# Performance work log

Hardware: AMD Instinct MI355X
Metric: run time of the kernel (lower is better)

## Reference

```python
import jax, jax.numpy as jnp
import numpy as np
from math import sqrt

B, N, M, HID, NH = 16, 512, 1024, 512, 8
HS = HID // NH  # 64


def layer_norm(x, g, b, eps=1e-5):
    mu = jnp.mean(x, axis=-1, keepdims=True)
    var = jnp.var(x, axis=-1, keepdims=True)
    return (x - mu) * jax.lax.rsqrt(var + eps) * g + b


def apply_moverz(x, s, c):
    # x: [B, L, NH, HS]; s, c: [B, L, 1, HS//2]
    x0, x1 = x[..., 0::2], x[..., 1::2]
    return jnp.concatenate([x0 * c - x1 * s, x1 * c + x0 * s], axis=-1)


def attention(q, k, v, mask):
    # q: [B,Nq,NH,HS], k/v: [B,Nk,NH,HS], mask broadcastable to [B,NH,Nq,Nk]
    attn = jnp.einsum('bnhd,bmhd->bhnm', q, k) / sqrt(HS)
    attn = jnp.where(mask, -jnp.inf, attn)
    attn = jax.nn.softmax(attn, axis=-1)
    x = jnp.einsum('bhnm,bmhd->bnhd', attn, v)
    return x.reshape(x.shape[0], x.shape[1], HID)


def setup_inputs() -> dict:
    key = jax.random.key(0)
    ks = jax.random.split(key, 24)
    inp = {}
    inp['tgt'] = jax.random.normal(ks[0], (B, N, HID), dtype=jnp.float32)
    inp['mem'] = jax.random.normal(ks[1], (B, M, HID), dtype=jnp.float32)
    th_p = jax.random.uniform(ks[2], (B, N, 1, HS // 2), dtype=jnp.float32) * (2 * np.pi)
    th_k = jax.random.uniform(ks[3], (B, M, 1, HS // 2), dtype=jnp.float32) * (2 * np.pi)
    inp['pep_mass_sin'] = jnp.sin(th_p)
    inp['pep_mass_cos'] = jnp.cos(th_p)
    inp['peaks_moverz_sin'] = jnp.sin(th_k)
    inp['peaks_moverz_cos'] = jnp.cos(th_k)
    # causal self-attn mask (True = masked)
    inp['tgt_mask'] = jnp.triu(jnp.ones((N, N), dtype=bool), k=1)[None, None]
    # pad last 64 memory positions
    pad = jnp.arange(M) >= (M - 64)
    inp['mem_key_padding_mask'] = jnp.broadcast_to(pad[None, None, None, :], (B, 1, 1, M))
    s = 0.02
    w = lambda i, shape: jax.random.normal(ks[i], shape, dtype=jnp.float32) * s
    # MaskedMultiHeadAttn params
    inp['mmha_w'] = w(4, (3 * HID, HID)); inp['mmha_b'] = jnp.zeros((3 * HID,), jnp.float32)
    inp['mmha_ow'] = w(5, (HID, HID)); inp['mmha_ob'] = jnp.zeros((HID,), jnp.float32)
    inp['mmha_g'] = jnp.ones((HID,), jnp.float32); inp['mmha_beta'] = jnp.zeros((HID,), jnp.float32)
    # MultiHeadAttn (cross) params
    inp['mha_qw'] = w(6, (HID, HID)); inp['mha_qb'] = jnp.zeros((HID,), jnp.float32)
    inp['mha_kvw'] = w(7, (2 * HID, HID)); inp['mha_kvb'] = jnp.zeros((2 * HID,), jnp.float32)
    inp['mha_ow'] = w(8, (HID, HID)); inp['mha_ob'] = jnp.zeros((HID,), jnp.float32)
    inp['mha_g'] = jnp.ones((HID,), jnp.float32); inp['mha_beta'] = jnp.zeros((HID,), jnp.float32)
    # FFN params (no bias)
    inp['ffn_w1'] = w(9, (4 * HID, HID))
    inp['ffn_w2'] = w(10, (HID, 4 * HID))
    inp['ffn_g'] = jnp.ones((HID,), jnp.float32); inp['ffn_beta'] = jnp.zeros((HID,), jnp.float32)
    return inp


def reference(tgt, mem, pep_mass_sin, pep_mass_cos, peaks_moverz_sin, peaks_moverz_cos,
              tgt_mask, mem_key_padding_mask,
              mmha_w, mmha_b, mmha_ow, mmha_ob, mmha_g, mmha_beta,
              mha_qw, mha_qb, mha_kvw, mha_kvb, mha_ow, mha_ob, mha_g, mha_beta,
              ffn_w1, ffn_w2, ffn_g, ffn_beta):
    # --- masked self-attention ---
    qkv = (tgt @ mmha_w.T + mmha_b).reshape(B, N, NH, 3 * HS)
    q, k, v = jnp.split(qkv, 3, axis=-1)
    x = attention(q, k, v, tgt_mask)
    tgt = layer_norm(x @ mmha_ow.T + mmha_ob + tgt, mmha_g, mmha_beta)
    # --- cross-attention with moverz distance bias ---
    q = (tgt @ mha_qw.T + mha_qb).reshape(B, N, NH, HS)
    q = apply_moverz(q, pep_mass_sin, pep_mass_cos)
    kv = (mem @ mha_kvw.T + mha_kvb).reshape(B, M, NH, 2 * HS)
    k, v = jnp.split(kv, 2, axis=-1)
    k = apply_moverz(k, peaks_moverz_sin, peaks_moverz_cos)
    x = attention(q, k, v, mem_key_padding_mask)
    tgt = layer_norm(x @ mha_ow.T + mha_ob + tgt, mha_g, mha_beta)
    # --- FFN ---
    h = jax.nn.relu(tgt @ ffn_w1.T) @ ffn_w2.T
    tgt = layer_norm(tgt + h, ffn_g, ffn_beta)
    return tgt
```

## Files before the change

kernel.cpp:

```cpp
#include <hip/hip_runtime.h>
#include <hip/hip_bf16.h>

#define BB 16
#define NN 512
#define MM 1024
#define HIDD 512
#define NHH 8

typedef unsigned short ushort_t;
typedef __attribute__((ext_vector_type(8))) short short8;
typedef __attribute__((ext_vector_type(8))) _Float16 half8;
typedef __attribute__((ext_vector_type(4))) _Float16 half4;
typedef __attribute__((ext_vector_type(4))) float f32x4;

__device__ __forceinline__ ushort_t f2bf(float x) {
    unsigned u = __float_as_uint(x);
    u += 0x7fff + ((u >> 16) & 1);
    return (ushort_t)(u >> 16);
}

#define GLD16(g, l) __builtin_amdgcn_global_load_lds(                      \
    (const __attribute__((address_space(1))) void*)(g),                    \
    (__attribute__((address_space(3))) void*)(l), 16, 0, 0)

__device__ __forceinline__ void xcd_swizzle(int& colb, int& rowb) {
    int id = blockIdx.x + blockIdx.y * gridDim.x;
    int C = gridDim.x;
    int xcd = id & 7;
    int slot = id >> 3;
    int rows_per = gridDim.y >> 3;
    colb = slot % C;
    rowb = xcd * rows_per + slot / C;
}

__global__ __launch_bounds__(256)
void gemm_bf(const ushort_t* __restrict__ A, const ushort_t* __restrict__ W,
             const float* __restrict__ bias, float* __restrict__ C,
             ushort_t* __restrict__ Cb, _Float16* __restrict__ Ch,
             int K, int Cout, int relu) {
    __shared__ __align__(16) ushort_t smem[2][8192];
    const int tid = threadIdx.x;
    const int lane = tid & 63;
    const int wid = tid >> 6;
    const int wm = wid >> 1, wn = wid & 1;
    int colb, rowb;
    xcd_swizzle(colb, rowb);
    const long row0 = (long)rowb * 128;
    const long col0 = (long)colb * 128;

    const int sr = lane >> 2;
    const int skq = lane & 3;
    const ushort_t* Ag = A + (row0 + wid * 32 + sr) * (long)K + skq * 8;
    const ushort_t* Wg = W + (col0 + wid * 32 + sr) * (long)K + skq * 8;
    const int sa0 = (wid * 32) * 32, sa1 = (wid * 32 + 16) * 32;

    f32x4 acc[4][4] = {};
    const int lr = lane & 15;
    const int kg = lane >> 4;

    GLD16(Ag, &smem[0][sa0]);
    GLD16(Ag + 16 * (long)K, &smem[0][sa1]);
    GLD16(Wg, &smem[0][4096 + sa0]);
    GLD16(Wg + 16 * (long)K, &smem[0][4096 + sa1]);

    int pb = 0;
    for (int k0 = 0; k0 < K; k0 += 32, pb ^= 1) {
        __syncthreads();
        int kn = k0 + 32;
        if (kn < K) {
            GLD16(Ag + kn, &smem[pb ^ 1][sa0]);
            GLD16(Ag + 16 * (long)K + kn, &smem[pb ^ 1][sa1]);
            GLD16(Wg + kn, &smem[pb ^ 1][4096 + sa0]);
            GLD16(Wg + 16 * (long)K + kn, &smem[pb ^ 1][4096 + sa1]);
        }
        const ushort_t* Ab = smem[pb];
        const ushort_t* Wb = smem[pb] + 4096;
        short8 af[4], bfr[4];
#pragma unroll
        for (int i = 0; i < 4; i++)
            af[i] = *(const short8*)&Ab[(wm * 64 + i * 16 + lr) * 32 + kg * 8];
#pragma unroll
        for (int j = 0; j < 4; j++)
            bfr[j] = *(const short8*)&Wb[(wn * 64 + j * 16 + lr) * 32 + kg * 8];
#pragma unroll
        for (int i = 0; i < 4; i++)
#pragma unroll
            for (int j = 0; j < 4; j++)
                acc[i][j] = __builtin_amdgcn_mfma_f32_16x16x32_bf16(
                    af[i], bfr[j], acc[i][j], 0, 0, 0);
    }

#pragma unroll
    for (int i = 0; i < 4; i++) {
#pragma unroll
        for (int j = 0; j < 4; j++) {
            long row = row0 + wm * 64 + i * 16 + kg * 4;
            long col = col0 + wn * 64 + j * 16 + lr;
            float bv = bias ? bias[col] : 0.f;
#pragma unroll
            for (int r = 0; r < 4; r++) {
                float x = acc[i][j][r] + bv;
                if (relu) x = fmaxf(x, 0.f);
                size_t idx = (row + r) * (size_t)Cout + col;
                if (Ch)      Ch[idx] = (_Float16)x;
                else if (Cb) Cb[idx] = f2bf(x);
                else         C[idx] = x;
            }
        }
    }
}

__global__ __launch_bounds__(256)
void gemm_bf64(const ushort_t* __restrict__ A, const ushort_t* __restrict__ W,
               const float* __restrict__ bias, float* __restrict__ C,
               ushort_t* __restrict__ Cb, _Float16* __restrict__ Ch,
               int K, int Cout, int relu) {
    __shared__ __align__(16) ushort_t smem[2][6144];
    const int tid = threadIdx.x;
    const int lane = tid & 63;
    const int w = tid >> 6;
    int colb, rowb;
    xcd_swizzle(colb, rowb);
    const long row0 = (long)rowb * 128;
    const long col0 = (long)colb * 64;

    const int sr = lane >> 2;
    const int skq = lane & 3;
    const ushort_t* Ag = A + (row0 + w * 32 + sr) * (long)K + skq * 8;
    const ushort_t* Wg = W + (col0 + w * 16 + sr) * (long)K + skq * 8;
    const int sa0 = (w * 32) * 32, sa1 = (w * 32 + 16) * 32;
    const int sw0 = 4096 + (w * 16) * 32;

    f32x4 acc[2][4] = {};
    const int lr = lane & 15;
    const int kg = lane >> 4;

    GLD16(Ag, &smem[0][sa0]);
    GLD16(Ag + 16 * (long)K, &smem[0][sa1]);
    GLD16(Wg, &smem[0][sw0]);

    int pb = 0;
    for (int k0 = 0; k0 < K; k0 += 32, pb ^= 1) {
        __syncthreads();
        int kn = k0 + 32;
        if (kn < K) {
            GLD16(Ag + kn, &smem[pb ^ 1][sa0]);
            GLD16(Ag + 16 * (long)K + kn, &smem[pb ^ 1][sa1]);
            GLD16(Wg + kn, &smem[pb ^ 1][sw0]);
        }
        const ushort_t* Ab = smem[pb];
        const ushort_t* Wb = smem[pb] + 4096;
        short8 af[2], bfr[4];
#pragma unroll
        for (int i = 0; i < 2; i++)
            af[i] = *(const short8*)&Ab[(w * 32 + i * 16 + lr) * 32 + kg * 8];
#pragma unroll
        for (int j = 0; j < 4; j++)
            bfr[j] = *(const short8*)&Wb[(j * 16 + lr) * 32 + kg * 8];
#pragma unroll
        for (int i = 0; i < 2; i++)
#pragma unroll
            for (int j = 0; j < 4; j++)
                acc[i][j] = __builtin_amdgcn_mfma_f32_16x16x32_bf16(
                    af[i], bfr[j], acc[i][j], 0, 0, 0);
    }

#pragma unroll
    for (int i = 0; i < 2; i++) {
#pragma unroll
        for (int j = 0; j < 4; j++) {
            long row = row0 + w * 32 + i * 16 + kg * 4;
            long col = col0 + j * 16 + lr;
            float bv = bias ? bias[col] : 0.f;
#pragma unroll
            for (int r = 0; r < 4; r++) {
                float x = acc[i][j][r] + bv;
                if (relu) x = fmaxf(x, 0.f);
                size_t idx = (row + r) * (size_t)Cout + col;
                if (Ch)      Ch[idx] = (_Float16)x;
                else if (Cb) Cb[idx] = f2bf(x);
                else         C[idx] = x;
            }
        }
    }
}

__global__ __launch_bounds__(256)
void gemm_q_rot(const ushort_t* __restrict__ A, const ushort_t* __restrict__ W,
                const float* __restrict__ bias,
                const float* __restrict__ sn, const float* __restrict__ cs,
                _Float16* __restrict__ Qrot) {
    __shared__ __align__(16) ushort_t smem[2][6144];
    _Float16* Cs = (_Float16*)smem;
    const int K = 512;
    const int tid = threadIdx.x;
    const int lane = tid & 63;
    const int w = tid >> 6;
    int colb, rowb;
    xcd_swizzle(colb, rowb);
    const long row0 = (long)rowb * 128;
    const int h = colb;
    const long col0 = (long)h * 64;

    const int sr = lane >> 2;
    const int skq = lane & 3;
    const ushort_t* Ag = A + (row0 + w * 32 + sr) * (long)K + skq * 8;
    const ushort_t* Wg = W + (col0 + w * 16 + sr) * (long)K + skq * 8;
    const int sa0 = (w * 32) * 32, sa1 = (w * 32 + 16) * 32;
    const int sw0 = 4096 + (w * 16) * 32;

    f32x4 acc[2][4] = {};
    const int lr = lane & 15;
    const int kg = lane >> 4;

    GLD16(Ag, &smem[0][sa0]);
    GLD16(Ag + 16 * (long)K, &smem[0][sa1]);
    GLD16(Wg, &smem[0][sw0]);

    int pb = 0;
    for (int k0 = 0; k0 < K; k0 += 32, pb ^= 1) {
        __syncthreads();
        int kn = k0 + 32;
        if (kn < K) {
            GLD16(Ag + kn, &smem[pb ^ 1][sa0]);
            GLD16(Ag + 16 * (long)K + kn, &smem[pb ^ 1][sa1]);
            GLD16(Wg + kn, &smem[pb ^ 1][sw0]);
        }
        const ushort_t* Ab = smem[pb];
        const ushort_t* Wb = smem[pb] + 4096;
        short8 af[2], bfr[4];
#pragma unroll
        for (int i = 0; i < 2; i++)
            af[i] = *(const short8*)&Ab[(w * 32 + i * 16 + lr) * 32 + kg * 8];
#pragma unroll
        for (int j = 0; j < 4; j++)
            bfr[j] = *(const short8*)&Wb[(j * 16 + lr) * 32 + kg * 8];
#pragma unroll
        for (int i = 0; i < 2; i++)
#pragma unroll
            for (int j = 0; j < 4; j++)
                acc[i][j] = __builtin_amdgcn_mfma_f32_16x16x32_bf16(
                    af[i], bfr[j], acc[i][j], 0, 0, 0);
    }

    __syncthreads();
#pragma unroll
    for (int i = 0; i < 2; i++)
#pragma unroll
        for (int j = 0; j < 4; j++) {
            int row = w * 32 + i * 16 + kg * 4;
            int col = j * 16 + lr;
            float bv = bias[col0 + col];
#pragma unroll
            for (int r = 0; r < 4; r++)
                Cs[(row + r) * 76 + col] = (_Float16)(acc[i][j][r] + bv);
        }
    __syncthreads();
    for (int idx = tid; idx < 4096; idx += 256) {
        int rr = idx >> 5, j = idx & 31;
        size_t srow = (size_t)row0 + rr;
        float x0 = (float)Cs[rr * 76 + 2 * j], x1 = (float)Cs[rr * 76 + 2 * j + 1];
        float s = sn[srow * 32 + j], c = cs[srow * 32 + j];
        Qrot[srow * 512 + h * 64 + j]      = (_Float16)(x0 * c - x1 * s);
        Qrot[srow * 512 + h * 64 + 32 + j] = (_Float16)(x1 * c + x0 * s);
    }
}

__global__ __launch_bounds__(256)
void gemm_kv(const ushort_t* __restrict__ A, const ushort_t* __restrict__ W,
             const float* __restrict__ bias,
             const float* __restrict__ sn, const float* __restrict__ cs,
             _Float16* __restrict__ Krot, _Float16* __restrict__ Vth) {
    __shared__ __align__(16) ushort_t smem[2][8192];
    _Float16* Cs = (_Float16*)smem;
    const int K = 512;
    const int tid = threadIdx.x;
    const int lane = tid & 63;
    const int wid = tid >> 6;
    const int wm = wid >> 1, wn = wid & 1;
    int colb, rowb;
    xcd_swizzle(colb, rowb);
    const long row0 = (long)rowb * 128;
    const int h = colb;
    const long col0 = (long)h * 128;

    const int sr = lane >> 2;
    const int skq = lane & 3;
    const ushort_t* Ag = A + (row0 + wid * 32 + sr) * (long)K + skq * 8;
    const ushort_t* Wg = W + (col0 + wid * 32 + sr) * (long)K + skq * 8;
    const int sa0 = (wid * 32) * 32, sa1 = (wid * 32 + 16) * 32;

    f32x4 acc[4][4] = {};
    const int lr = lane & 15;
    const int kg = lane >> 4;

    GLD16(Ag, &smem[0][sa0]);
    GLD16(Ag + 16 * (long)K, &smem[0][sa1]);
    GLD16(Wg, &smem[0][4096 + sa0]);
    GLD16(Wg + 16 * (long)K, &smem[0][4096 + sa1]);

    int pb = 0;
    for (int k0 = 0; k0 < K; k0 += 32, pb ^= 1) {
        __syncthreads();
        int kn = k0 + 32;
        if (kn < K) {
            GLD16(Ag + kn, &smem[pb ^ 1][sa0]);
            GLD16(Ag + 16 * (long)K + kn, &smem[pb ^ 1][sa1]);
            GLD16(Wg + kn, &smem[pb ^ 1][4096 + sa0]);
            GLD16(Wg + 16 * (long)K + kn, &smem[pb ^ 1][4096 + sa1]);
        }
        const ushort_t* Ab = smem[pb];
        const ushort_t* Wb = smem[pb] + 4096;
        short8 af[4], bfr[4];
#pragma unroll
        for (int i = 0; i < 4; i++)
            af[i] = *(const short8*)&Ab[(wm * 64 + i * 16 + lr) * 32 + kg * 8];
#pragma unroll
        for (int j = 0; j < 4; j++)
            bfr[j] = *(const short8*)&Wb[(wn * 64 + j * 16 + lr) * 32 + kg * 8];
#pragma unroll
        for (int i = 0; i < 4; i++)
#pragma unroll
            for (int j = 0; j < 4; j++)
                acc[i][j] = __builtin_amdgcn_mfma_f32_16x16x32_bf16(
                    af[i], bfr[j], acc[i][j], 0, 0, 0);
    }

    const int b_ = (int)(row0 >> 10);
    const int m0_ = (int)(row0 & 1023);
#pragma unroll
    for (int half = 0; half < 2; half++) {
        __syncthreads();
        if (wn == half) {
#pragma unroll
            for (int i = 0; i < 4; i++)
#pragma unroll
                for (int j = 0; j < 4; j++) {
                    int row = wm * 64 + i * 16 + kg * 4;
                    int col = j * 16 + lr;
                    float bv = bias[col0 + half * 64 + col];
#pragma unroll
                    for (int r = 0; r < 4; r++)
                        Cs[(row + r) * 76 + col] = (_Float16)(acc[i][j][r] + bv);
                }
        }
        __syncthreads();
        if (half == 0) {
            for (int idx = tid; idx < 4096; idx += 256) {
                int rr = idx >> 5, j = idx & 31;
                size_t srow = (size_t)row0 + rr;
                float x0 = (float)Cs[rr * 76 + 2 * j], x1 = (float)Cs[rr * 76 + 2 * j + 1];
                float s = sn[srow * 32 + j], c = cs[srow * 32 + j];
                Krot[srow * 512 + h * 64 + j]      = (_Float16)(x0 * c - x1 * s);
                Krot[srow * 512 + h * 64 + 32 + j] = (_Float16)(x1 * c + x0 * s);
            }
        } else {
            for (int idx = tid; idx < 1024; idx += 256) {
                int d = idx >> 4, c = idx & 15;
                half8 v;
#pragma unroll
                for (int k = 0; k < 8; k++) v[k] = Cs[(c * 8 + k) * 76 + d];
                *(half8*)(Vth + (((size_t)(b_ * NHH + h)) * 64 + d) * MM
                          + m0_ + c * 8) = v;
            }
        }
    }
}

__global__ __launch_bounds__(256)
void cvt_all(const float* __restrict__ tgt, const float* __restrict__ mem,
             const float* __restrict__ w0, const float* __restrict__ w1,
             const float* __restrict__ w2, const float* __restrict__ w3,
             const float* __restrict__ w4, const float* __restrict__ w5,
             const float* __restrict__ w6,
             ushort_t* __restrict__ Abf, ushort_t* __restrict__ membf,
             ushort_t* __restrict__ Wbf) {
    int blk = blockIdx.x;
    const float* src;
    ushort_t* dst;
    size_t off;
    if (blk < 4096)       { src = tgt; dst = Abf;   off = (size_t)blk * 1024; }
    else if (blk < 12288) { src = mem; dst = membf; off = (size_t)(blk - 4096) * 1024; }
    else {
        int wb = blk - 12288;
        dst = Wbf + (size_t)wb * 1024;
        if (wb < 768)       { src = w0; off = (size_t)wb * 1024; }
        else if (wb < 1024) { src = w1; off = (size_t)(wb - 768) * 1024; }
        else if (wb < 1280) { src = w2; off = (size_t)(wb - 1024) * 1024; }
        else if (wb < 1792) { src = w3; off = (size_t)(wb - 1280) * 1024; }
        else if (wb < 2048) { src = w4; off = (size_t)(wb - 1792) * 1024; }
        else if (wb < 3072) { src = w5; off = (size_t)(wb - 2048) * 1024; }
        else                { src = w6; off = (size_t)(wb - 3072) * 1024; }
        float4 v = *(const float4*)(src + off + threadIdx.x * 4);
        ushort4 o;
        o.x = f2bf(v.x); o.y = f2bf(v.y); o.z = f2bf(v.z); o.w = f2bf(v.w);
        *(ushort4*)(dst + threadIdx.x * 4) = o;
        return;
    }
    float4 v = *(const float4*)(src + off + threadIdx.x * 4);
    ushort4 o;
    o.x = f2bf(v.x); o.y = f2bf(v.y); o.z = f2bf(v.z); o.w = f2bf(v.w);
    *(ushort4*)(dst + off + threadIdx.x * 4) = o;
}

__global__ __launch_bounds__(256)
void prep_vt(const _Float16* __restrict__ src, int L, int stride,
             int hmul, int hadd, _Float16* __restrict__ Vt) {
    const int b = blockIdx.z, h = blockIdx.y, m0 = blockIdx.x * 64;
    const int tid = threadIdx.x;
    __shared__ _Float16 vt[64][72];
    for (int idx = tid; idx < 512; idx += 256) {
        int m = idx >> 3, c = idx & 7;
        half8 v = *(const half8*)(src + ((size_t)(b * L + m0 + m)) * stride
                                  + h * hmul + hadd + c * 8);
#pragma unroll
        for (int k = 0; k < 8; k++) vt[c * 8 + k][m] = v[k];
    }
    __syncthreads();
    for (int idx = tid; idx < 512; idx += 256) {
        int d = idx >> 3, c = idx & 7;
        *(half8*)(Vt + (((size_t)(b * NHH + h)) * 64 + d) * L + m0 + c * 8)
            = *(const half8*)&vt[d][c * 8];
    }
}

__global__ __launch_bounds__(256)
void attn7(const _Float16* __restrict__ Q, int qstride, int qmul, int qadd,
           const _Float16* __restrict__ K, int kstride, int kmul, int kadd,
           const _Float16* __restrict__ Vt, int LV, int Lrows,
           ushort_t* __restrict__ out, int kvlen, int causal) {
    const int g = blockIdx.x;
    const int bh = (g & 7) * 16 + ((g >> 3) & 15);
    const int qb = g >> 7;
    const int b = bh >> 3, h = bh & 7;
    const int n0 = qb * 128;
    const int tid = threadIdx.x, lane = tid & 63, w = tid >> 6;
    const int quad = lane >> 4, l16 = lane & 15;
    const int qw = n0 + w * 32;

    __shared__ _Float16 Ks[64 * 64];
    __shared__ _Float16 Vs[64 * 64];
    __shared__ _Float16 Ps[4][32 * 64];
    _Float16* Pw = Ps[w];

    half8 bq[2][2];
#pragma unroll
    for (int s = 0; s < 2; s++)
#pragma unroll
        for (int c = 0; c < 2; c++)
            bq[s][c] = *(const half8*)(Q + ((size_t)(b * NN + qw + s * 16 + l16)) * qstride
                                       + h * qmul + qadd + c * 32 + quad * 8);

    f32x4 acc[2][4] = {};
    float mrun[2] = {-3e38f, -3e38f}, lrun[2] = {0.f, 0.f};

    const int srow = tid >> 3;
    const int scol = tid & 7;
    const int ssw = (scol ^ (srow & 7)) * 8;
    const int limit = causal ? (n0 + 128) : kvlen;

    half8 kr0, kr1, vr0, vr1;
    {
        size_t kb = ((size_t)(b * Lrows + srow)) * kstride + h * kmul + kadd + scol * 8;
        kr0 = *(const half8*)(K + kb);
        kr1 = *(const half8*)(K + kb + (size_t)32 * kstride);
        size_t vb = (((size_t)(b * NHH + h)) * 64 + srow) * (size_t)LV + scol * 8;
        vr0 = *(const half8*)(Vt + vb);
        vr1 = *(const half8*)(Vt + vb + (size_t)32 * LV);
    }

    const int fsw = l16 & 7;
    for (int key0 = 0; key0 < limit; key0 += 64) {
        __syncthreads();
        *(half8*)&Ks[srow * 64 + ssw] = kr0;
        *(half8*)&Ks[(srow + 32) * 64 + ssw] = kr1;
        *(half8*)&Vs[srow * 64 + ssw] = vr0;
        *(half8*)&Vs[(srow + 32) * 64 + ssw] = vr1;
        __syncthreads();
        int knext = key0 + 64;
        if (knext < limit) {
            size_t kb = ((size_t)(b * Lrows + knext + srow)) * kstride
                        + h * kmul + kadd + scol * 8;
            kr0 = *(const half8*)(K + kb);
            kr1 = *(const half8*)(K + kb + (size_t)32 * kstride);
            size_t vb = (((size_t)(b * NHH + h)) * 64 + srow) * (size_t)LV
                        + knext + scol * 8;
            vr0 = *(const half8*)(Vt + vb);
            vr1 = *(const half8*)(Vt + vb + (size_t)32 * LV);
        }
        if (causal && key0 > qw + 31) continue;

        f32x4 st[2][4];
#pragma unroll
        for (int kt = 0; kt < 4; kt++) {
            const int rk = kt * 16 + l16;
            half8 ak0 = *(const half8*)&Ks[rk * 64 + ((quad ^ fsw) * 8)];
            half8 ak1 = *(const half8*)&Ks[rk * 64 + (((quad + 4) ^ fsw) * 8)];
#pragma unroll
            for (int s = 0; s < 2; s++) {
                f32x4 z = {};
                z = __builtin_amdgcn_mfma_f32_16x16x32_f16(ak0, bq[s][0], z, 0, 0, 0);
                z = __builtin_amdgcn_mfma_f32_16x16x32_f16(ak1, bq[s][1], z, 0, 0, 0);
                st[s][kt] = z;
            }
        }
        if (causal && key0 + 64 > qw) {
#pragma unroll
            for (int s = 0; s < 2; s++) {
                int qabs = qw + s * 16 + l16;
#pragma unroll
                for (int kt = 0; kt < 4; kt++)
#pragma unroll
                    for (int r = 0; r < 4; r++)
                        if (key0 + kt * 16 + quad * 4 + r > qabs)
                            st[s][kt][r] = -3e38f;
            }
        }
#pragma unroll
        for (int s = 0; s < 2; s++) {
            float lm = -3e38f;
#pragma unroll
            for (int kt = 0; kt < 4; kt++)
                lm = fmaxf(lm, fmaxf(fmaxf(st[s][kt][0], st[s][kt][1]),
                                     fmaxf(st[s][kt][2], st[s][kt][3])));
            lm = fmaxf(lm, __shfl_xor(lm, 16));
            lm = fmaxf(lm, __shfl_xor(lm, 32));
            float mnew = fmaxf(mrun[s], lm);
            float corr = __expf((mrun[s] - mnew) * 0.125f);
            mrun[s] = mnew;
            float ls = 0.f;
            const int rp = s * 16 + l16;
#pragma unroll
            for (int kt = 0; kt < 4; kt++) {
                half4 ph;
#pragma unroll
                for (int r = 0; r < 4; r++) {
                    float p = __expf((st[s][kt][r] - mnew) * 0.125f);
                    ls += p;
                    ph[r] = (_Float16)p;
                }
                int jc = 2 * kt + (quad >> 1);
                *(half4*)&Pw[rp * 64 + ((jc ^ fsw) * 8) + (quad & 1) * 4] = ph;
            }
            ls += __shfl_xor(ls, 16);
            ls += __shfl_xor(ls, 32);
            lrun[s] = lrun[s] * corr + ls;
            float cb0 = __shfl(corr, (lane & 48) | (quad * 4 + 0));
            float cb1 = __shfl(corr, (lane & 48) | (quad * 4 + 1));
            float cb2 = __shfl(corr, (lane & 48) | (quad * 4 + 2));
            float cb3 = __shfl(corr, (lane & 48) | (quad * 4 + 3));
#pragma unroll
            for (int dt = 0; dt < 4; dt++) {
                acc[s][dt][0] *= cb0; acc[s][dt][1] *= cb1;
                acc[s][dt][2] *= cb2; acc[s][dt][3] *= cb3;
            }
        }
        half8 ap[2][2];
#pragma unroll
        for (int s = 0; s < 2; s++) {
            const int rp = s * 16 + l16;
#pragma unroll
            for (int c = 0; c < 2; c++)
                ap[s][c] = *(const half8*)&Pw[rp * 64 + (((c * 4 + quad) ^ fsw) * 8)];
        }
#pragma unroll
        for (int dt = 0; dt < 4; dt++) {
            const int rv = dt * 16 + l16;
            half8 bv0 = *(const half8*)&Vs[rv * 64 + ((quad ^ fsw) * 8)];
            half8 bv1 = *(const half8*)&Vs[rv * 64 + (((quad + 4) ^ fsw) * 8)];
#pragma unroll
            for (int s = 0; s < 2; s++) {
                acc[s][dt] = __builtin_amdgcn_mfma_f32_16x16x32_f16(ap[s][0], bv0, acc[s][dt], 0, 0, 0);
                acc[s][dt] = __builtin_amdgcn_mfma_f32_16x16x32_f16(ap[s][1], bv1, acc[s][dt], 0, 0, 0);
            }
        }
    }
#pragma unroll
    for (int s = 0; s < 2; s++) {
        float invq = 1.f / lrun[s];
        float iv0 = __shfl(invq, (lane & 48) | (quad * 4 + 0));
        float iv1 = __shfl(invq, (lane & 48) | (quad * 4 + 1));
        float iv2 = __shfl(invq, (lane & 48) | (quad * 4 + 2));
        float iv3 = __shfl(invq, (lane & 48) | (quad * 4 + 3));
#pragma unroll
        for (int dt = 0; dt < 4; dt++) {
            size_t base = ((size_t)(b * NN + qw + s * 16 + quad * 4)) * 512
                          + h * 64 + dt * 16 + l16;
            out[base]           = f2bf(acc[s][dt][0] * iv0);
            out[base + 512]     = f2bf(acc[s][dt][1] * iv1);
            out[base + 1024]    = f2bf(acc[s][dt][2] * iv2);
            out[base + 1536]    = f2bf(acc[s][dt][3] * iv3);
        }
    }
}

__global__ __launch_bounds__(256)
void ln_residual(const float* __restrict__ u, int nsplit,
                 const float* __restrict__ res,
                 const float* __restrict__ g, const float* __restrict__ be,
                 float* __restrict__ out, ushort_t* __restrict__ outbf) {
    const int row = blockIdx.x, t = threadIdx.x;
    const float* rp = res + (size_t)row * HIDD;
    float z0 = rp[t];
    float z1 = rp[t + 256];
    for (int s = 0; s < nsplit; s++) {
        const float* up = u + (size_t)s * 4194304 + (size_t)row * HIDD;
        z0 += up[t];
        z1 += up[t + 256];
    }
    float sm = z0 + z1, s2 = z0 * z0 + z1 * z1;
#pragma unroll
    for (int off = 1; off < 64; off <<= 1) {
        sm += __shfl_xor(sm, off, 64);
        s2 += __shfl_xor(s2, off, 64);
    }
    __shared__ float ps[4], ps2[4];
    int w = t >> 6;
    if ((t & 63) == 0) { ps[w] = sm; ps2[w] = s2; }
    __syncthreads();
    sm = ps[0] + ps[1] + ps[2] + ps[3];
    s2 = ps2[0] + ps2[1] + ps2[2] + ps2[3];
    float mu = sm * (1.f / 512.f);
    float var = s2 * (1.f / 512.f) - mu * mu;
    float rstd = rsqrtf(var + 1e-5f);
    float y0 = (z0 - mu) * rstd * g[t] + be[t];
    float y1 = (z1 - mu) * rstd * g[t + 256] + be[t + 256];
    out[(size_t)row * HIDD + t]       = y0;
    out[(size_t)row * HIDD + t + 256] = y1;
    if (outbf) {
        outbf[(size_t)row * HIDD + t]       = f2bf(y0);
        outbf[(size_t)row * HIDD + t + 256] = f2bf(y1);
    }
}

extern "C" void kernel_launch(void* const* d_in, const int* in_sizes, int n_in,
                              void* d_out, int out_size, void* d_ws, size_t ws_size,
                              hipStream_t stream) {
    const float* tgt      = (const float*)d_in[0];
    const float* mem      = (const float*)d_in[1];
    const float* pep_sin  = (const float*)d_in[2];
    const float* pep_cos  = (const float*)d_in[3];
    const float* pk_sin   = (const float*)d_in[4];
    const float* pk_cos   = (const float*)d_in[5];
    const float* mmha_w   = (const float*)d_in[8];
    const float* mmha_b   = (const float*)d_in[9];
    const float* mmha_ow  = (const float*)d_in[10];
    const float* mmha_ob  = (const float*)d_in[11];
    const float* mmha_g   = (const float*)d_in[12];
    const float* mmha_be  = (const float*)d_in[13];
    const float* mha_qw   = (const float*)d_in[14];
    const float* mha_qb   = (const float*)d_in[15];
    const float* mha_kvw  = (const float*)d_in[16];
    const float* mha_kvb  = (const float*)d_in[17];
    const float* mha_ow   = (const float*)d_in[18];
    const float* mha_ob   = (const float*)d_in[19];
    const float* mha_g    = (const float*)d_in[20];
    const float* mha_be   = (const float*)d_in[21];
    const float* ffn_w1   = (const float*)d_in[22];
    const float* ffn_w2   = (const float*)d_in[23];
    const float* ffn_g    = (const float*)d_in[24];
    const float* ffn_be   = (const float*)d_in[25];

    float* ws = (float*)d_ws;
    float* utmp  = ws;
    float* tgt12 = ws + 4194304;
    _Float16* hp = (_Float16*)(ws + 8388608);
    _Float16* qkvh  = hp;
    _Float16* Qrot  = hp + 12582912;
    _Float16* Vth   = hp + 16777216;
    _Float16* Krot  = hp + 25165824;
    ushort_t* membf = (ushort_t*)(hp + 33554432);
    ushort_t* Abf   = (ushort_t*)(hp + 41943040);
    ushort_t* Wbf   = (ushort_t*)(hp + 46137344);
    ushort_t* w_mmha = Wbf;
    ushort_t* w_mmow = Wbf + 786432;
    ushort_t* w_qw   = Wbf + 1048576;
    ushort_t* w_kvw  = Wbf + 1310720;
    ushort_t* w_mow  = Wbf + 1835008;
    ushort_t* w_f1   = Wbf + 2097152;
    ushort_t* w_f2   = Wbf + 3145728;
    ushort_t* hbf = (ushort_t*)qkvh;
    float* out = (float*)d_out;
    (void)in_sizes; (void)n_in; (void)out_size; (void)ws_size;

    cvt_all<<<16384, 256, 0, stream>>>(tgt, mem, mmha_w, mmha_ow, mha_qw,
                                       mha_kvw, mha_ow, ffn_w1, ffn_w2,
                                       Abf, membf, Wbf);
    gemm_bf<<<dim3(12, 64), 256, 0, stream>>>(Abf, w_mmha, mmha_b, nullptr, nullptr, qkvh, 512, 1536, 0);
    prep_vt<<<dim3(8, NHH, BB), 256, 0, stream>>>(qkvh, NN, 1536, 192, 128, Vth);
    attn7<<<512, 256, 0, stream>>>(qkvh, 1536, 192, 0, qkvh, 1536, 192, 64,
                                   Vth, NN, NN, Abf, 0, 1);
    gemm_bf64<<<dim3(8, 64), 256, 0, stream>>>(Abf, w_mmow, mmha_ob, utmp, nullptr, nullptr, 512, 512, 0);
    ln_residual<<<8192, 256, 0, stream>>>(utmp, 1, tgt, mmha_g, mmha_be, tgt12, Abf);
    gemm_q_rot<<<dim3(8, 64), 256, 0, stream>>>(Abf, w_qw, mha_qb, pep_sin, pep_cos, Qrot);
    gemm_kv<<<dim3(8, 128), 256, 0, stream>>>(membf, w_kvw, mha_kvb, pk_sin, pk_cos, Krot, Vth);
    attn7<<<512, 256, 0, stream>>>(Qrot, 512, 64, 0, Krot, 512, 64, 0,
                                   Vth, MM, MM, Abf, MM - 64, 0);
    gemm_bf64<<<dim3(8, 64), 256, 0, stream>>>(Abf, w_mow, mha_ob, utmp, nullptr, nullptr, 512, 512, 0);
    ln_residual<<<8192, 256, 0, stream>>>(utmp, 1, tgt12, mha_g, mha_be, tgt12, Abf);
    gemm_bf<<<dim3(16, 64), 256, 0, stream>>>(Abf, w_f1, nullptr, nullptr, hbf, nullptr, 512, 2048, 1);
    gemm_bf64<<<dim3(8, 64), 256, 0, stream>>>(hbf, w_f2, nullptr, utmp, nullptr, nullptr, 2048, 512, 0);
    ln_residual<<<8192, 256, 0, stream>>>(utmp, 1, tgt12, ffn_g, ffn_be, out, nullptr);
}
```

Measured before the change: 405.6 us.

## Restructure attention to 8 waves, double-buffered K/V LDS, lazy rescale and exp2

The attention kernel now uses 512 threads and 8 waves, each handling 16 query rows instead of 32. K/V tiles are double-buffered in LDS so only one barrier per tile is needed, with register prefetch two tiles ahead. Softmax switches to exp2 with a folded scale, and the running max is only updated when it grows by more than a threshold, which skips most accumulator rescales. s_setprio is placed around the MFMA sections. The trade-off is more LDS per block, less register reuse of each K/V fragment per wave, and a risk of fp16 overflow in P if the lazy-max threshold lets values grow too large.

```diff
diff --git a/kernel.cpp b/kernel.cpp
--- a/kernel.cpp
+++ b/kernel.cpp
@@ -424,8 +424,8 @@
     }
 }
 
-__global__ __launch_bounds__(256)
-void attn7(const _Float16* __restrict__ Q, int qstride, int qmul, int qadd,
+__global__ __launch_bounds__(512, 4)
+void attn8(const _Float16* __restrict__ Q, int qstride, int qmul, int qadd,
            const _Float16* __restrict__ K, int kstride, int kmul, int kadd,
            const _Float16* __restrict__ Vt, int LV, int Lrows,
            ushort_t* __restrict__ out, int kvlen, int causal) {
@@ -436,161 +436,158 @@
     const int n0 = qb * 128;
     const int tid = threadIdx.x, lane = tid & 63, w = tid >> 6;
     const int quad = lane >> 4, l16 = lane & 15;
-    const int qw = n0 + w * 32;
-
-    __shared__ _Float16 Ks[64 * 64];
-    __shared__ _Float16 Vs[64 * 64];
-    __shared__ _Float16 Ps[4][32 * 64];
+    const int qw = n0 + w * 16;
+
+    __shared__ _Float16 Ks[2][64 * 64];
+    __shared__ _Float16 Vs[2][64 * 64];
+    __shared__ _Float16 Ps[8][16 * 64];
     _Float16* Pw = Ps[w];
 
-    half8 bq[2][2];
-#pragma unroll
-    for (int s = 0; s < 2; s++)
-#pragma unroll
-        for (int c = 0; c < 2; c++)
-            bq[s][c] = *(const half8*)(Q + ((size_t)(b * NN + qw + s * 16 + l16)) * qstride
-                                       + h * qmul + qadd + c * 32 + quad * 8);
-
-    f32x4 acc[2][4] = {};
-    float mrun[2] = {-3e38f, -3e38f}, lrun[2] = {0.f, 0.f};
+    half8 bq[2];
+#pragma unroll
+    for (int c = 0; c < 2; c++)
+        bq[c] = *(const half8*)(Q + ((size_t)(b * NN + qw + l16)) * qstride
+                                + h * qmul + qadd + c * 32 + quad * 8);
+
+    f32x4 acc[4] = {};
+    float mrun = -3e38f, lrun = 0.f;
 
     const int srow = tid >> 3;
     const int scol = tid & 7;
     const int ssw = (scol ^ (srow & 7)) * 8;
+
     const int limit = causal ? (n0 + 128) : kvlen;
-
-    half8 kr0, kr1, vr0, vr1;
-    {
-        size_t kb = ((size_t)(b * Lrows + srow)) * kstride + h * kmul + kadd + scol * 8;
-        kr0 = *(const half8*)(K + kb);
-        kr1 = *(const half8*)(K + kb + (size_t)32 * kstride);
-        size_t vb = (((size_t)(b * NHH + h)) * 64 + srow) * (size_t)LV + scol * 8;
-        vr0 = *(const half8*)(Vt + vb);
-        vr1 = *(const half8*)(Vt + vb + (size_t)32 * LV);
-    }
-
+    const int nt = limit >> 6;
+
+    const size_t kbase = ((size_t)(b * Lrows)) * kstride + h * kmul + kadd;
+    const size_t vbase = (((size_t)(b * NHH + h)) * 64 + srow) * (size_t)LV;
+
+    half8 kr = *(const half8*)(K + kbase + (size_t)srow * kstride + scol * 8);
+    half8 vr = *(const half8*)(Vt + vbase + scol * 8);
+    *(half8*)&Ks[0][srow * 64 + ssw] = kr;
+    *(half8*)&Vs[0][srow * 64 + ssw] = vr;
+    if (nt > 1) {
+        kr = *(const half8*)(K + kbase + (size_t)(64 + srow) * kstride + scol * 8);
+        vr = *(const half8*)(Vt + vbase + 64 + scol * 8);
+    }
+
+    const float SC = 0.125f * 1.44269504f;
     const int fsw = l16 & 7;
-    for (int key0 = 0; key0 < limit; key0 += 64) {
+    int pb = 0;
+    for (int t = 0; t < nt; t++, pb ^= 1) {
+        const int key0 = t * 64;
         __syncthreads();
-        *(half8*)&Ks[srow * 64 + ssw] = kr0;
-        *(half8*)&Ks[(srow + 32) * 64 + ssw] = kr1;
-        *(half8*)&Vs[srow * 64 + ssw] = vr0;
-        *(half8*)&Vs[(srow + 32) * 64 + ssw] = vr1;
-        __syncthreads();
-        int knext = key0 + 64;
-        if (knext < limit) {
-            size_t kb = ((size_t)(b * Lrows + knext + srow)) * kstride
-                        + h * kmul + kadd + scol * 8;
-            kr0 = *(const half8*)(K + kb);
-            kr1 = *(const half8*)(K + kb + (size_t)32 * kstride);
-            size_t vb = (((size_t)(b * NHH + h)) * 64 + srow) * (size_t)LV
-                        + knext + scol * 8;
-            vr0 = *(const half8*)(Vt + vb);
-            vr1 = *(const half8*)(Vt + vb + (size_t)32 * LV);
-        }
-        if (causal && key0 > qw + 31) continue;
-
-        f32x4 st[2][4];
+        if (t + 1 < nt) {
+            *(half8*)&Ks[pb ^ 1][srow * 64 + ssw] = kr;
+            *(half8*)&Vs[pb ^ 1][srow * 64 + ssw] = vr;
+            if (t + 2 < nt) {
+                kr = *(const half8*)(K + kbase
+                        + (size_t)((t + 2) * 64 + srow) * kstride + scol * 8);
+                vr = *(const half8*)(Vt + vbase + (t + 2) * 64 + scol * 8);
+            }
+        }
+        if (causal && key0 > qw + 15) continue;
+
+        const _Float16* Kb = Ks[pb];
+        const _Float16* Vb = Vs[pb];
+        f32x4 st[4];
+        __builtin_amdgcn_s_setprio(1);
 #pragma unroll
         for (int kt = 0; kt < 4; kt++) {
             const int rk = kt * 16 + l16;
-            half8 ak0 = *(const half8*)&Ks[rk * 64 + ((quad ^ fsw) * 8)];
-            half8 ak1 = *(const half8*)&Ks[rk * 64 + (((quad + 4) ^ fsw) * 8)];
-#pragma unroll
-            for (int s = 0; s < 2; s++) {
-                f32x4 z = {};
-                z = __builtin_amdgcn_mfma_f32_16x16x32_f16(ak0, bq[s][0], z, 0, 0, 0);
-                z = __builtin_amdgcn_mfma_f32_16x16x32_f16(ak1, bq[s][1], z, 0, 0, 0);
-                st[s][kt] = z;
+            half8 ak0 = *(const half8*)&Kb[rk * 64 + ((quad ^ fsw) * 8)];
+            half8 ak1 = *(const half8*)&Kb[rk * 64 + (((quad + 4) ^ fsw) * 8)];
+            f32x4 z = {};
+            z = __builtin_amdgcn_mfma_f32_16x16x32_f16(ak0, bq[0], z, 0, 0, 0);
+            z = __builtin_amdgcn_mfma_f32_16x16x32_f16(ak1, bq[1], z, 0, 0, 0);
+            st[kt] = z;
+        }
+        __builtin_amdgcn_s_setprio(0);
+
+        if (causal && key0 + 64 > qw) {
+            const int qabs = qw + l16;
+#pragma unroll
+            for (int kt = 0; kt < 4; kt++)
+#pragma unroll
+                for (int r = 0; r < 4; r++)
+                    if (key0 + kt * 16 + quad * 4 + r > qabs)
+                        st[kt][r] = -3e38f;
+        }
+
+        float lm = -3e38f;
+#pragma unroll
+        for (int kt = 0; kt < 4; kt++)
+            lm = fmaxf(lm, fmaxf(fmaxf(st[kt][0], st[kt][1]),
+                                 fmaxf(st[kt][2], st[kt][3])));
+        lm = fmaxf(lm, __shfl_xor(lm, 16));
+        lm = fmaxf(lm, __shfl_xor(lm, 32));
+
+        const int keep = __all(lm - mrun <= 64.f);
+        float corr = 0.f;
+        if (!keep) {
+            float mnew = fmaxf(mrun, lm);
+            corr = exp2f((mrun - mnew) * SC);
+            mrun = mnew;
+        }
+        const float mb = mrun * SC;
+        float ls = 0.f;
+#pragma unroll
+        for (int kt = 0; kt < 4; kt++) {
+            half4 ph;
+#pragma unroll
+            for (int r = 0; r < 4; r++) {
+                float p = exp2f(__builtin_fmaf(st[kt][r], SC, -mb));
+                ls += p;
+                ph[r] = (_Float16)p;
             }
-        }
-        if (causal && key0 + 64 > qw) {
-#pragma unroll
-            for (int s = 0; s < 2; s++) {
-                int qabs = qw + s * 16 + l16;
-#pragma unroll
-                for (int kt = 0; kt < 4; kt++)
-#pragma unroll
-                    for (int r = 0; r < 4; r++)
-                        if (key0 + kt * 16 + quad * 4 + r > qabs)
-                            st[s][kt][r] = -3e38f;
-            }
-        }
-#pragma unroll
-        for (int s = 0; s < 2; s++) {
-            float lm = -3e38f;
-#pragma unroll
-            for (int kt = 0; kt < 4; kt++)
-                lm = fmaxf(lm, fmaxf(fmaxf(st[s][kt][0], st[s][kt][1]),
-                                     fmaxf(st[s][kt][2], st[s][kt][3])));
-            lm = fmaxf(lm, __shfl_xor(lm, 16));
-            lm = fmaxf(lm, __shfl_xor(lm, 32));
-            float mnew = fmaxf(mrun[s], lm);
-            float corr = __expf((mrun[s] - mnew) * 0.125f);
-            mrun[s] = mnew;
-            float ls = 0.f;
-            const int rp = s * 16 + l16;
-#pragma unroll
-            for (int kt = 0; kt < 4; kt++) {
-                half4 ph;
-#pragma unroll
-                for (int r = 0; r < 4; r++) {
-                    float p = __expf((st[s][kt][r] - mnew) * 0.125f);
-                    ls += p;
-                    ph[r] = (_Float16)p;
-                }
-                int jc = 2 * kt + (quad >> 1);
-                *(half4*)&Pw[rp * 64 + ((jc ^ fsw) * 8) + (quad & 1) * 4] = ph;
-            }
-            ls += __shfl_xor(ls, 16);
-            ls += __shfl_xor(ls, 32);
-            lrun[s] = lrun[s] * corr + ls;
+            int jc = 2 * kt + (quad >> 1);
+            *(half4*)&Pw[l16 * 64 + ((jc ^ fsw) * 8) + (quad & 1) * 4] = ph;
+        }
+        ls += __shfl_xor(ls, 16);
+        ls += __shfl_xor(ls, 32);
+        if (keep) {
+            lrun += ls;
+        } else {
+            lrun = lrun * corr + ls;
             float cb0 = __shfl(corr, (lane & 48) | (quad * 4 + 0));
             float cb1 = __shfl(corr, (lane & 48) | (quad * 4 + 1));
             float cb2 = __shfl(corr, (lane & 48) | (quad * 4 + 2));
             float cb3 = __shfl(corr, (lane & 48) | (quad * 4 + 3));
 #pragma unroll
             for (int dt = 0; dt < 4; dt++) {
-                acc[s][dt][0] *= cb0; acc[s][dt][1] *= cb1;
-                acc[s][dt][2] *= cb2; acc[s][dt][3] *= cb3;
+                acc[dt][0] *= cb0; acc[dt][1] *= cb1;
+                acc[dt][2] *= cb2; acc[dt][3] *= cb3;
             }
         }
-        half8 ap[2][2];
-#pragma unroll
-        for (int s = 0; s < 2; s++) {
-            const int rp = s * 16 + l16;
-#pragma unroll
-            for (int c = 0; c < 2; c++)
-                ap[s][c] = *(const half8*)&Pw[rp * 64 + (((c * 4 + quad) ^ fsw) * 8)];
-        }
+        half8 ap[2];
+#pragma unroll
+        for (int c = 0; c < 2; c++)
+            ap[c] = *(const half8*)&Pw[l16 * 64 + (((c * 4 + quad) ^ fsw) * 8)];
+        __builtin_amdgcn_s_setprio(1);
 #pragma unroll
         for (int dt = 0; dt < 4; dt++) {
             const int rv = dt * 16 + l16;
-            half8 bv0 = *(const half8*)&Vs[rv * 64 + ((quad ^ fsw) * 8)];
-            half8 bv1 = *(const half8*)&Vs[rv * 64 + (((quad + 4) ^ fsw) * 8)];
-#pragma unroll
-            for (int s = 0; s < 2; s++) {
-                acc[s][dt] = __builtin_amdgcn_mfma_f32_16x16x32_f16(ap[s][0], bv0, acc[s][dt], 0, 0, 0);
-                acc[s][dt] = __builtin_amdgcn_mfma_f32_16x16x32_f16(ap[s][1], bv1, acc[s][dt], 0, 0, 0);
-            }
-        }
-    }
-#pragma unroll
-    for (int s = 0; s < 2; s++) {
-        float invq = 1.f / lrun[s];
-        float iv0 = __shfl(invq, (lane & 48) | (quad * 4 + 0));
-        float iv1 = __shfl(invq, (lane & 48) | (quad * 4 + 1));
-        float iv2 = __shfl(invq, (lane & 48) | (quad * 4 + 2));
-        float iv3 = __shfl(invq, (lane & 48) | (quad * 4 + 3));
-#pragma unroll
-        for (int dt = 0; dt < 4; dt++) {
-            size_t base = ((size_t)(b * NN + qw + s * 16 + quad * 4)) * 512
-                          + h * 64 + dt * 16 + l16;
-            out[base]           = f2bf(acc[s][dt][0] * iv0);
-            out[base + 512]     = f2bf(acc[s][dt][1] * iv1);
-            out[base + 1024]    = f2bf(acc[s][dt][2] * iv2);
-            out[base + 1536]    = f2bf(acc[s][dt][3] * iv3);
-        }
+            half8 bv0 = *(const half8*)&Vb[rv * 64 + ((quad ^ fsw) * 8)];
+            half8 bv1 = *(const half8*)&Vb[rv * 64 + (((quad + 4) ^ fsw) * 8)];
+            acc[dt] = __builtin_amdgcn_mfma_f32_16x16x32_f16(ap[0], bv0, acc[dt], 0, 0, 0);
+            acc[dt] = __builtin_amdgcn_mfma_f32_16x16x32_f16(ap[1], bv1, acc[dt], 0, 0, 0);
+        }
+        __builtin_amdgcn_s_setprio(0);
+    }
+
+    float invq = 1.f / lrun;
+    float iv0 = __shfl(invq, (lane & 48) | (quad * 4 + 0));
+    float iv1 = __shfl(invq, (lane & 48) | (quad * 4 + 1));
+    float iv2 = __shfl(invq, (lane & 48) | (quad * 4 + 2));
+    float iv3 = __shfl(invq, (lane & 48) | (quad * 4 + 3));
+#pragma unroll
+    for (int dt = 0; dt < 4; dt++) {
+        size_t base = ((size_t)(b * NN + qw + quad * 4)) * 512
+                      + h * 64 + dt * 16 + l16;
+        out[base]           = f2bf(acc[dt][0] * iv0);
+        out[base + 512]     = f2bf(acc[dt][1] * iv1);
+        out[base + 1024]    = f2bf(acc[dt][2] * iv2);
+        out[base + 1536]    = f2bf(acc[dt][3] * iv3);
     }
 }
 
@@ -688,13 +685,13 @@
                                        Abf, membf, Wbf);
     gemm_bf<<<dim3(12, 64), 256, 0, stream>>>(Abf, w_mmha, mmha_b, nullptr, nullptr, qkvh, 512, 1536, 0);
     prep_vt<<<dim3(8, NHH, BB), 256, 0, stream>>>(qkvh, NN, 1536, 192, 128, Vth);
-    attn7<<<512, 256, 0, stream>>>(qkvh, 1536, 192, 0, qkvh, 1536, 192, 64,
+    attn8<<<512, 512, 0, stream>>>(qkvh, 1536, 192, 0, qkvh, 1536, 192, 64,
                                    Vth, NN, NN, Abf, 0, 1);
     gemm_bf64<<<dim3(8, 64), 256, 0, stream>>>(Abf, w_mmow, mmha_ob, utmp, nullptr, nullptr, 512, 512, 0);
     ln_residual<<<8192, 256, 0, stream>>>(utmp, 1, tgt, mmha_g, mmha_be, tgt12, Abf);
     gemm_q_rot<<<dim3(8, 64), 256, 0, stream>>>(Abf, w_qw, mha_qb, pep_sin, pep_cos, Qrot);
     gemm_kv<<<dim3(8, 128), 256, 0, stream>>>(membf, w_kvw, mha_kvb, pk_sin, pk_cos, Krot, Vth);
-    attn7<<<512, 256, 0, stream>>>(Qrot, 512, 64, 0, Krot, 512, 64, 0,
+    attn8<<<512, 512, 0, stream>>>(Qrot, 512, 64, 0, Krot, 512, 64, 0,
                                    Vth, MM, MM, Abf, MM - 64, 0);
     gemm_bf64<<<dim3(8, 64), 256, 0, stream>>>(Abf, w_mow, mha_ob, utmp, nullptr, nullptr, 512, 512, 0);
     ln_residual<<<8192, 256, 0, stream>>>(utmp, 1, tgt12, mha_g, mha_be, tgt12, Abf);
```

Measured after the change: 399.5 us. No clear change (-1.5%).
